# Kernel tuning notes

Hardware: AMD Instinct MI355X
Metric: run time of the kernel (lower is better)

Reference implementation:

```python
import jax, jax.numpy as jnp
import numpy as np

D_MODEL = 1024
D_FF = 4096
N_EXPERTS = 8
TOP_K = 2
GATE_TEMP = 1.0
LOAD_BALANCE_WEIGHT = 0.01


def setup_inputs() -> dict:
    key = jax.random.key(0)
    ks = jax.random.split(key, 6)
    B, S = 4, 2048
    x = jax.random.normal(ks[0], (B, S, D_MODEL), dtype=jnp.float32)
    # gate: nn.Linear(d_model, n_experts, bias=False), weight ~ N(0, 0.1)
    gate_w = 0.1 * jax.random.normal(ks[1], (N_EXPERTS, D_MODEL), dtype=jnp.float32)
    # stacked expert weights (stored as [in, out] for x @ W)
    s1 = 1.0 / np.sqrt(D_MODEL)
    s2 = 1.0 / np.sqrt(D_FF)
    W1 = jax.random.uniform(ks[2], (N_EXPERTS, D_MODEL, D_FF), jnp.float32, -s1, s1)
    b1 = jax.random.uniform(ks[3], (N_EXPERTS, D_FF), jnp.float32, -s1, s1)
    W2 = jax.random.uniform(ks[4], (N_EXPERTS, D_FF, D_MODEL), jnp.float32, -s2, s2)
    b2 = jax.random.uniform(ks[5], (N_EXPERTS, D_MODEL), jnp.float32, -s2, s2)
    return {"x": x, "gate_w": gate_w, "W1": W1, "b1": b1, "W2": W2, "b2": b2}


def reference(x, gate_w, W1, b1, W2, b2):
    B, S, D = x.shape
    E = gate_w.shape[0]
    xf = x.reshape(-1, D)                                  # [N, D]
    logits = (xf @ gate_w.T) / GATE_TEMP                   # [N, E]
    gate_probs = jax.nn.softmax(logits, axis=-1)           # [N, E]
    topk_probs, topk_idx = jax.lax.top_k(gate_probs, TOP_K)
    topk_probs = topk_probs / jnp.sum(topk_probs, axis=-1, keepdims=True)
    # per-token combine weight for each expert: [N, E]
    combine = jnp.einsum("nk,nke->ne", topk_probs,
                         jax.nn.one_hot(topk_idx, E, dtype=xf.dtype))
    out = jnp.zeros_like(xf)
    for e in range(E):  # fixed small loop over experts (structurally distinct weights)
        h = jax.nn.gelu(xf @ W1[e] + b1[e], approximate=False)  # [N, d_ff]
        out = out + combine[:, e:e + 1] * (h @ W2[e] + b2[e])
    out = out.reshape(B, S, D)
    # auxiliary load-balance loss (faithful: softmax probs > 0 almost surely)
    prob_mean = jnp.mean(gate_probs, axis=0)
    tokens_per_expert = jnp.mean((gate_probs > 0).astype(xf.dtype), axis=0)
    aux_loss = jnp.sum(prob_mean * tokens_per_expert) * E * LOAD_BALANCE_WEIGHT
    return out, aux_loss
```

## Files before the change

### kernel.cpp

```cpp
#include <hip/hip_runtime.h>
#include <cstdint>

typedef unsigned short u16;
typedef __attribute__((ext_vector_type(8))) __bf16 bf16x8;
typedef __attribute__((ext_vector_type(4))) float f32x4;

#define NTOK 8192
#define DM   1024
#define DFF  4096
#define NE   8
#define NT_MAX 136

typedef const __attribute__((address_space(1))) unsigned gl_u32;
typedef __attribute__((address_space(3))) unsigned lds_u32;

static __device__ __forceinline__ u16 f2bf(float f) {
    union { float f; unsigned u; } v; v.f = f;
    unsigned r = v.u + 0x7fffu + ((v.u >> 16) & 1u);
    return (u16)(r >> 16);
}

__global__ __launch_bounds__(256) void transpose_cvt_kernel(const float* __restrict__ W,
                                                            u16* __restrict__ WT,
                                                            int K, int F) {
    __shared__ float tile[64][33];
    size_t eo = (size_t)blockIdx.z * K * F;
    const float* src = W + eo;
    u16* dst = WT + eo;
    int k0 = blockIdx.y * 64, f0 = blockIdx.x * 32;
    int tid = threadIdx.x;
    {
        int rk = tid >> 2, cf = (tid & 3) * 8;
        const float* s = src + (size_t)(k0 + rk) * F + f0 + cf;
        f32x4 v0 = *(const f32x4*)(s);
        f32x4 v1 = *(const f32x4*)(s + 4);
#pragma unroll
        for (int i = 0; i < 4; i++) { tile[rk][cf + i] = v0[i]; tile[rk][cf + 4 + i] = v1[i]; }
    }
    __syncthreads();
    {
        int f = tid >> 3, kq = (tid & 7) * 8;
        union { ushort4 h[2]; uint4 q; } o;
#pragma unroll
        for (int i = 0; i < 8; i++) {
            u16 b = f2bf(tile[kq + i][f]);
            ((u16*)&o)[i] = b;
        }
        *(uint4*)(dst + (size_t)(f0 + f) * K + k0 + kq) = o.q;
    }
}

__global__ __launch_bounds__(256) void gate_kernel(const float* __restrict__ x,
                                                   const float* __restrict__ gw,
                                                   u16* __restrict__ xb,
                                                   int* __restrict__ cnt,
                                                   float* __restrict__ psum,
                                                   float* __restrict__ indsum,
                                                   int* __restrict__ list,
                                                   float* __restrict__ wgt,
                                                   int4* __restrict__ tokIE,
                                                   float2* __restrict__ tokW) {
    __shared__ float s_psum[NE], s_ind[NE];
    __shared__ int s_cnt[NE], s_base[NE];
    __shared__ int s_tok[NE][32];
    __shared__ float s_wgt[NE][32];
    __shared__ int s_e1[32], s_p1[32], s_e2[32], s_p2[32];
    __shared__ float s_w1[32], s_w2[32];
    int tid = threadIdx.x, lane = tid & 63, wid = tid >> 6;
    if (tid < NE) { s_psum[tid] = 0.f; s_ind[tid] = 0.f; s_cnt[tid] = 0; }
    __syncthreads();
#pragma unroll 1
    for (int it = 0; it < 8; it++) {
        int t = blockIdx.x * 32 + wid * 8 + it;
        const float* xr = x + (size_t)t * DM;
        float xv[16];
#pragma unroll
        for (int i = 0; i < 4; i++) {
            f32x4 v = *(const f32x4*)(xr + i * 256 + lane * 4);
            xv[4 * i + 0] = v[0]; xv[4 * i + 1] = v[1];
            xv[4 * i + 2] = v[2]; xv[4 * i + 3] = v[3];
            ushort4 o;
            o.x = f2bf(v[0]); o.y = f2bf(v[1]); o.z = f2bf(v[2]); o.w = f2bf(v[3]);
            *(ushort4*)(xb + (size_t)t * DM + i * 256 + lane * 4) = o;
        }
        float p[NE];
#pragma unroll
        for (int e = 0; e < NE; e++) {
            const float* gr = gw + (size_t)e * DM;
            float d = 0.f;
#pragma unroll
            for (int i = 0; i < 4; i++) {
                f32x4 g = *(const f32x4*)(gr + i * 256 + lane * 4);
                d += xv[4 * i] * g[0] + xv[4 * i + 1] * g[1]
                   + xv[4 * i + 2] * g[2] + xv[4 * i + 3] * g[3];
            }
#pragma unroll
            for (int off = 32; off; off >>= 1) d += __shfl_xor(d, off);
            p[e] = d;
        }
        float m = p[0];
#pragma unroll
        for (int e = 1; e < NE; e++) m = fmaxf(m, p[e]);
        float s = 0.f;
#pragma unroll
        for (int e = 0; e < NE; e++) { p[e] = expf(p[e] - m); s += p[e]; }
        float inv = 1.f / s;
#pragma unroll
        for (int e = 0; e < NE; e++) p[e] *= inv;
        int i1 = 0; float p1 = p[0];
#pragma unroll
        for (int e = 1; e < NE; e++) if (p[e] > p1) { p1 = p[e]; i1 = e; }
        int i2 = (i1 == 0) ? 1 : 0; float p2 = p[i2];
#pragma unroll
        for (int e = 0; e < NE; e++) if (e != i1 && p[e] > p2) { p2 = p[e]; i2 = e; }
        float wnorm = 1.f / (p1 + p2);
        if (lane == 0) {
#pragma unroll
            for (int e = 0; e < NE; e++) {
                atomicAdd(&s_psum[e], p[e]);
                atomicAdd(&s_ind[e], (p[e] > 0.f) ? 1.f : 0.f);
            }
            int pos1 = atomicAdd(&s_cnt[i1], 1);
            s_tok[i1][pos1] = t; s_wgt[i1][pos1] = p1 * wnorm;
            int pos2 = atomicAdd(&s_cnt[i2], 1);
            s_tok[i2][pos2] = t; s_wgt[i2][pos2] = p2 * wnorm;
            int sl = wid * 8 + it;
            s_e1[sl] = i1; s_p1[sl] = pos1; s_w1[sl] = p1 * wnorm;
            s_e2[sl] = i2; s_p2[sl] = pos2; s_w2[sl] = p2 * wnorm;
        }
    }
    __syncthreads();
    if (tid < NE) {
        s_base[tid] = atomicAdd(&cnt[tid], s_cnt[tid]);
        atomicAdd(&psum[tid], s_psum[tid]);
        atomicAdd(&indsum[tid], s_ind[tid]);
    }
    __syncthreads();
    for (int idx = tid; idx < NE * 32; idx += 256) {
        int e = idx >> 5, j = idx & 31;
        if (j < s_cnt[e]) {
            list[e * NTOK + s_base[e] + j] = s_tok[e][j];
            wgt[e * NTOK + s_base[e] + j] = s_wgt[e][j];
        }
    }
    if (tid < 32) {
        int t = blockIdx.x * 32 + tid;
        int e1 = s_e1[tid], e2 = s_e2[tid];
        tokIE[t] = make_int4(e1, s_base[e1] + s_p1[tid], e2, s_base[e2] + s_p2[tid]);
        tokW[t] = make_float2(s_w1[tid], s_w2[tid]);
    }
}

__global__ void finalize_kernel(const float* __restrict__ psum,
                                const float* __restrict__ indsum,
                                const int* __restrict__ cnt,
                                int* __restrict__ baseArr,
                                int* __restrict__ tileE,
                                int* __restrict__ tileM0,
                                int* __restrict__ nTiles,
                                float* __restrict__ out_aux) {
    if (threadIdx.x == 0) {
        float a = 0.f; int b = 0, nt = 0;
        for (int e = 0; e < NE; e++) {
            a += (psum[e] * (1.f / NTOK)) * (indsum[e] * (1.f / NTOK));
            baseArr[e] = b; b += cnt[e];
            int mt = (cnt[e] + 127) >> 7;
            for (int i = 0; i < mt; i++) { tileE[nt] = e; tileM0[nt] = i; nt++; }
        }
        nTiles[0] = nt;
        out_aux[0] = a * (float)NE * 0.01f;
    }
}

template <int KDIM, int EPI>
__global__ __launch_bounds__(256, 4) void gemm_kernel(const u16* __restrict__ A,
                                                      const u16* __restrict__ BT,
                                                      const float* __restrict__ bias,
                                                      const int* __restrict__ list,
                                                      const float* __restrict__ wgt,
                                                      const int* __restrict__ cnt,
                                                      const int* __restrict__ base,
                                                      const int* __restrict__ tileE,
                                                      const int* __restrict__ tileM0,
                                                      const int* __restrict__ nTiles,
                                                      u16* __restrict__ h_out,
                                                      float* __restrict__ out) {
    constexpr int NCOL = (EPI == 1) ? DFF : DM;
    constexpr int NY = NCOL / 128;
    constexpr int NT = KDIM / 64;
    constexpr int BAND = 4 * NY;
    int nwg = gridDim.x;
    int q = nwg >> 3, r = nwg & 7;
    int xcd = blockIdx.x & 7, idx0 = blockIdx.x >> 3;
    int wg = (xcd < r ? xcd * (q + 1) : r * (q + 1) + (xcd - r) * q) + idx0;
    int band = wg / BAND, ib = wg - band * BAND;
    int ny = ib >> 2;
    int t = band * 4 + (ib & 3);
    if (t >= nTiles[0]) return;
    int e = tileE[t];
    int m0 = tileM0[t] << 7;
    int M = cnt[e];
    int hb = base[e];
    int n0 = ny * 128;
    const int* le = list + e * NTOK;
    const float* we = wgt + e * NTOK;
    const u16* Bte = BT + (size_t)e * NCOL * KDIM;
    const float* be = bias + (size_t)e * NCOL;

    __shared__ __attribute__((aligned(16))) u16 lA[128 * 64];
    __shared__ __attribute__((aligned(16))) u16 lB[128 * 64];

    int tid = threadIdx.x;
    int lane = tid & 63, wid = tid >> 6;
    int wr = wid >> 1, wc = wid & 1;
    int r16 = lane & 15, hi = lane >> 4;
    int r8 = r16 & 7;

    const u16* aG[4]; const u16* bG[4]; int lofs[4];
#pragma unroll
    for (int qq = 0; qq < 4; qq++) {
        int lin = qq * 256 + tid;
        int row = lin >> 3, j = lin & 7;
        int js = j ^ (row & 7);
        lofs[qq] = lin * 8;
        int pos = m0 + row; if (pos > M - 1) pos = M - 1;
        size_t arow = (EPI == 1) ? (size_t)le[pos] : (size_t)(hb + pos);
        aG[qq] = A + arow * KDIM + js * 8;
        bG[qq] = Bte + (size_t)(n0 + row) * KDIM + js * 8;
    }

#define STAGE(k0)                                                                   \
    do {                                                                            \
        _Pragma("unroll")                                                           \
        for (int qq = 0; qq < 4; qq++) {                                            \
            __builtin_amdgcn_global_load_lds((gl_u32*)(aG[qq] + (k0)),              \
                (lds_u32*)(lA + lofs[qq]), 16, 0, 0);                               \
            __builtin_amdgcn_global_load_lds((gl_u32*)(bG[qq] + (k0)),              \
                (lds_u32*)(lB + lofs[qq]), 16, 0, 0);                               \
        }                                                                           \
    } while (0)

    f32x4 acc[4][4];
#pragma unroll
    for (int m = 0; m < 4; m++)
#pragma unroll
        for (int n = 0; n < 4; n++) acc[m][n] = (f32x4){0.f, 0.f, 0.f, 0.f};

    STAGE(0);

#pragma unroll 1
    for (int tI = 0; tI < NT; ++tI) {
        asm volatile("s_waitcnt vmcnt(0)" ::: "memory");
        __builtin_amdgcn_s_barrier();
#pragma unroll
        for (int kk = 0; kk < 2; kk++) {
            bf16x8 aF[4], bF[4];
            int ch = ((kk << 2) | hi) ^ r8;
#pragma unroll
            for (int m = 0; m < 4; m++)
                aF[m] = *(const bf16x8*)(lA + ((wr * 64 + m * 16 + r16) << 6) + (ch << 3));
#pragma unroll
            for (int n = 0; n < 4; n++)
                bF[n] = *(const bf16x8*)(lB + ((wc * 64 + n * 16 + r16) << 6) + (ch << 3));
            __builtin_amdgcn_s_setprio(1);
#pragma unroll
            for (int m = 0; m < 4; m++)
#pragma unroll
                for (int n = 0; n < 4; n++)
                    acc[m][n] = __builtin_amdgcn_mfma_f32_16x16x32_bf16(aF[m], bF[n], acc[m][n], 0, 0, 0);
            __builtin_amdgcn_s_setprio(0);
        }
        asm volatile("s_waitcnt lgkmcnt(0)" ::: "memory");
        __builtin_amdgcn_s_barrier();
        if (tI + 1 < NT) STAGE((tI + 1) * 64);
    }
#undef STAGE

#pragma unroll
    for (int m = 0; m < 4; m++) {
        int pr = m0 + wr * 64 + m * 16 + hi * 4;
#pragma unroll
        for (int n = 0; n < 4; n++) {
            int f = n0 + wc * 64 + n * 16 + r16;
#pragma unroll
            for (int j = 0; j < 4; j++) {
                int p = pr + j;
                if (p < M) {
                    if constexpr (EPI == 1) {
                        float v = acc[m][n][j] + be[f];
                        float ex = __expf(v * (1.5957691216f + 0.0713548162f * v * v));
                        v = v - v / (ex + 1.0f);
                        h_out[(size_t)(hb + p) * DFF + f] = f2bf(v);
                    } else if constexpr (EPI == 2) {
                        out[(size_t)(hb + p) * DM + f] = acc[m][n][j];
                    } else {
                        atomicAdd(out + (size_t)le[p] * DM + f,
                                  we[p] * (acc[m][n][j] + be[f]));
                    }
                }
            }
        }
    }
}

__global__ __launch_bounds__(256) void combine_kernel(const float* __restrict__ pairOut,
                                                      const float* __restrict__ b2,
                                                      const int4* __restrict__ tokIE,
                                                      const float2* __restrict__ tokW,
                                                      const int* __restrict__ baseArr,
                                                      float* __restrict__ out) {
    int t = blockIdx.x;
    int c = threadIdx.x * 4;
    int4 ie = tokIE[t];
    float2 w = tokW[t];
    int s1 = baseArr[ie.x] + ie.y, s2 = baseArr[ie.z] + ie.w;
    f32x4 v1 = *(const f32x4*)(pairOut + (size_t)s1 * DM + c);
    f32x4 v2 = *(const f32x4*)(pairOut + (size_t)s2 * DM + c);
    f32x4 g1 = *(const f32x4*)(b2 + (size_t)ie.x * DM + c);
    f32x4 g2 = *(const f32x4*)(b2 + (size_t)ie.z * DM + c);
    f32x4 res = w.x * (v1 + g1) + w.y * (v2 + g2);
    *(f32x4*)(out + (size_t)t * DM + c) = res;
}

extern "C" void kernel_launch(void* const* d_in, const int* in_sizes, int n_in,
                              void* d_out, int out_size, void* d_ws, size_t ws_size,
                              hipStream_t stream) {
    const float* x  = (const float*)d_in[0];
    const float* gw = (const float*)d_in[1];
    const float* W1 = (const float*)d_in[2];
    const float* b1 = (const float*)d_in[3];
    const float* W2 = (const float*)d_in[4];
    const float* b2 = (const float*)d_in[5];
    float* out = (float*)d_out;

    char* ws = (char*)d_ws;
    size_t o_xb   = 0;
    size_t o_w1t  = (size_t)16 << 20;
    size_t o_w2t  = o_w1t + ((size_t)64 << 20);
    size_t o_h    = o_w2t + ((size_t)64 << 20);
    size_t o_pair = o_h + ((size_t)128 << 20);
    size_t ctrl_sz = (size_t)1 << 20;
    bool pair_path = ws_size >= o_pair + ((size_t)64 << 20) + ctrl_sz;
    size_t o_ctrl = pair_path ? (o_pair + ((size_t)64 << 20)) : o_pair;

    u16* xb   = (u16*)(ws + o_xb);
    u16* w1t  = (u16*)(ws + o_w1t);
    u16* w2t  = (u16*)(ws + o_w2t);
    u16* h    = (u16*)(ws + o_h);
    float* pairOut = (float*)(ws + o_pair);
    char* ctrl = ws + o_ctrl;
    int*    cnt     = (int*)ctrl;
    float*  psum    = (float*)(ctrl + 32);
    float*  indsum  = (float*)(ctrl + 64);
    int*    baseArr = (int*)(ctrl + 96);
    int*    list    = (int*)(ctrl + 192);
    float*  wgt     = (float*)(ctrl + 192 + 262144);
    int4*   tokIE   = (int4*)(ctrl + 192 + 524288);
    float2* tokW    = (float2*)(ctrl + 192 + 655360);
    int*    tileE   = (int*)(ctrl + 192 + 720896);
    int*    tileM0  = (int*)(ctrl + 192 + 724992);
    int*    nTiles  = (int*)(ctrl + 192 + 729088);

    (void)hipMemsetAsync(ctrl, 0, 192, stream);
    if (!pair_path)
        (void)hipMemsetAsync(d_out, 0, (size_t)out_size * sizeof(float), stream);

    transpose_cvt_kernel<<<dim3(DFF / 32, DM / 64, NE), 256, 0, stream>>>(W1, w1t, DM, DFF);
    transpose_cvt_kernel<<<dim3(DM / 32, DFF / 64, NE), 256, 0, stream>>>(W2, w2t, DFF, DM);
    gate_kernel<<<NTOK / 32, 256, 0, stream>>>(x, gw, xb, cnt, psum, indsum, list, wgt, tokIE, tokW);
    finalize_kernel<<<1, 64, 0, stream>>>(psum, indsum, cnt, baseArr, tileE, tileM0, nTiles,
                                          out + (size_t)NTOK * DM);

    gemm_kernel<DM, 1><<<dim3(NT_MAX * (DFF / 128)), 256, 0, stream>>>(
        xb, w1t, b1, list, wgt, cnt, baseArr, tileE, tileM0, nTiles, h, nullptr);
    if (pair_path) {
        gemm_kernel<DFF, 2><<<dim3(NT_MAX * (DM / 128)), 256, 0, stream>>>(
            h, w2t, b2, list, wgt, cnt, baseArr, tileE, tileM0, nTiles, nullptr, pairOut);
        combine_kernel<<<NTOK, 256, 0, stream>>>(pairOut, b2, tokIE, tokW, baseArr, out);
    } else {
        gemm_kernel<DFF, 3><<<dim3(NT_MAX * (DM / 128)), 256, 0, stream>>>(
            h, w2t, b2, list, wgt, cnt, baseArr, tileE, tileM0, nTiles, nullptr, out);
    }
}
```

Measured before the change: 535.3 us.

## Split second expert GEMM along K into two halves and sum in combine

The down-projection GEMM is split-K by two: each tile is handled by two workgroups covering half of the 4096-long reduction, writing to separate partial buffers. The combine kernel adds both partials before applying bias and routing weights. This doubles the number of workgroups for the second GEMM, which otherwise has relatively few tiles for the GPU. The cost is an extra partial-output buffer (reusing the W1-transpose workspace region) plus extra reads in combine.

New measurement: 537.8 us. No clear change (+0.5%).

```diff
diff --git a/kernel.cpp b/kernel.cpp
--- a/kernel.cpp
+++ b/kernel.cpp
@@ -172,7 +172,7 @@
     }
 }
 
-template <int KDIM, int EPI>
+template <int KSTRIDE, int KLEN, int EPI>
 __global__ __launch_bounds__(256, 4) void gemm_kernel(const u16* __restrict__ A,
                                                       const u16* __restrict__ BT,
                                                       const float* __restrict__ bias,
@@ -184,15 +184,18 @@
                                                       const int* __restrict__ tileM0,
                                                       const int* __restrict__ nTiles,
                                                       u16* __restrict__ h_out,
-                                                      float* __restrict__ out) {
+                                                      float* __restrict__ out,
+                                                      float* __restrict__ out2) {
     constexpr int NCOL = (EPI == 1) ? DFF : DM;
     constexpr int NY = NCOL / 128;
-    constexpr int NT = KDIM / 64;
+    constexpr int NT = KLEN / 64;
     constexpr int BAND = 4 * NY;
     int nwg = gridDim.x;
     int q = nwg >> 3, r = nwg & 7;
     int xcd = blockIdx.x & 7, idx0 = blockIdx.x >> 3;
     int wg = (xcd < r ? xcd * (q + 1) : r * (q + 1) + (xcd - r) * q) + idx0;
+    int kh = 0;
+    if constexpr (EPI == 2) { kh = wg & 1; wg >>= 1; }
     int band = wg / BAND, ib = wg - band * BAND;
     int ny = ib >> 2;
     int t = band * 4 + (ib & 3);
@@ -202,9 +205,10 @@
     int M = cnt[e];
     int hb = base[e];
     int n0 = ny * 128;
+    int kOff = kh * KLEN;
     const int* le = list + e * NTOK;
     const float* we = wgt + e * NTOK;
-    const u16* Bte = BT + (size_t)e * NCOL * KDIM;
+    const u16* Bte = BT + (size_t)e * NCOL * KSTRIDE;
     const float* be = bias + (size_t)e * NCOL;
 
     __shared__ __attribute__((aligned(16))) u16 lA[128 * 64];
@@ -225,8 +229,8 @@
         lofs[qq] = lin * 8;
         int pos = m0 + row; if (pos > M - 1) pos = M - 1;
         size_t arow = (EPI == 1) ? (size_t)le[pos] : (size_t)(hb + pos);
-        aG[qq] = A + arow * KDIM + js * 8;
-        bG[qq] = Bte + (size_t)(n0 + row) * KDIM + js * 8;
+        aG[qq] = A + arow * KSTRIDE + kOff + js * 8;
+        bG[qq] = Bte + (size_t)(n0 + row) * KSTRIDE + kOff + js * 8;
     }
 
 #define STAGE(k0)                                                                   \
@@ -276,6 +280,7 @@
     }
 #undef STAGE
 
+    float* dst = (EPI == 2 && kh) ? out2 : out;
 #pragma unroll
     for (int m = 0; m < 4; m++) {
         int pr = m0 + wr * 64 + m * 16 + hi * 4;
@@ -292,7 +297,7 @@
                         v = v - v / (ex + 1.0f);
                         h_out[(size_t)(hb + p) * DFF + f] = f2bf(v);
                     } else if constexpr (EPI == 2) {
-                        out[(size_t)(hb + p) * DM + f] = acc[m][n][j];
+                        dst[(size_t)(hb + p) * DM + f] = acc[m][n][j];
                     } else {
                         atomicAdd(out + (size_t)le[p] * DM + f,
                                   we[p] * (acc[m][n][j] + be[f]));
@@ -303,7 +308,8 @@
     }
 }
 
-__global__ __launch_bounds__(256) void combine_kernel(const float* __restrict__ pairOut,
+__global__ __launch_bounds__(256) void combine_kernel(const float* __restrict__ pairA,
+                                                      const float* __restrict__ pairB,
                                                       const float* __restrict__ b2,
                                                       const int4* __restrict__ tokIE,
                                                       const float2* __restrict__ tokW,
@@ -314,11 +320,13 @@
     int4 ie = tokIE[t];
     float2 w = tokW[t];
     int s1 = baseArr[ie.x] + ie.y, s2 = baseArr[ie.z] + ie.w;
-    f32x4 v1 = *(const f32x4*)(pairOut + (size_t)s1 * DM + c);
-    f32x4 v2 = *(const f32x4*)(pairOut + (size_t)s2 * DM + c);
+    f32x4 a1 = *(const f32x4*)(pairA + (size_t)s1 * DM + c);
+    f32x4 b1v = *(const f32x4*)(pairB + (size_t)s1 * DM + c);
+    f32x4 a2 = *(const f32x4*)(pairA + (size_t)s2 * DM + c);
+    f32x4 b2v = *(const f32x4*)(pairB + (size_t)s2 * DM + c);
     f32x4 g1 = *(const f32x4*)(b2 + (size_t)ie.x * DM + c);
     f32x4 g2 = *(const f32x4*)(b2 + (size_t)ie.z * DM + c);
-    f32x4 res = w.x * (v1 + g1) + w.y * (v2 + g2);
+    f32x4 res = w.x * (a1 + b1v + g1) + w.y * (a2 + b2v + g2);
     *(f32x4*)(out + (size_t)t * DM + c) = res;
 }
 
@@ -347,7 +355,8 @@
     u16* w1t  = (u16*)(ws + o_w1t);
     u16* w2t  = (u16*)(ws + o_w2t);
     u16* h    = (u16*)(ws + o_h);
-    float* pairOut = (float*)(ws + o_pair);
+    float* pairA = (float*)(ws + o_pair);
+    float* pairB = (float*)(ws + o_w1t);
     char* ctrl = ws + o_ctrl;
     int*    cnt     = (int*)ctrl;
     float*  psum    = (float*)(ctrl + 32);
@@ -371,14 +380,14 @@
     finalize_kernel<<<1, 64, 0, stream>>>(psum, indsum, cnt, baseArr, tileE, tileM0, nTiles,
                                           out + (size_t)NTOK * DM);
 
-    gemm_kernel<DM, 1><<<dim3(NT_MAX * (DFF / 128)), 256, 0, stream>>>(
-        xb, w1t, b1, list, wgt, cnt, baseArr, tileE, tileM0, nTiles, h, nullptr);
+    gemm_kernel<DM, DM, 1><<<dim3(NT_MAX * (DFF / 128)), 256, 0, stream>>>(
+        xb, w1t, b1, list, wgt, cnt, baseArr, tileE, tileM0, nTiles, h, nullptr, nullptr);
     if (pair_path) {
-        gemm_kernel<DFF, 2><<<dim3(NT_MAX * (DM / 128)), 256, 0, stream>>>(
-            h, w2t, b2, list, wgt, cnt, baseArr, tileE, tileM0, nTiles, nullptr, pairOut);
-        combine_kernel<<<NTOK, 256, 0, stream>>>(pairOut, b2, tokIE, tokW, baseArr, out);
+        gemm_kernel<DFF, DFF / 2, 2><<<dim3(NT_MAX * (DM / 128) * 2), 256, 0, stream>>>(
+            h, w2t, b2, list, wgt, cnt, baseArr, tileE, tileM0, nTiles, nullptr, pairA, pairB);
+        combine_kernel<<<NTOK, 256, 0, stream>>>(pairA, pairB, b2, tokIE, tokW, baseArr, out);
     } else {
-        gemm_kernel<DFF, 3><<<dim3(NT_MAX * (DM / 128)), 256, 0, stream>>>(
-            h, w2t, b2, list, wgt, cnt, baseArr, tileE, tileM0, nTiles, nullptr, out);
-    }
-}
+        gemm_kernel<DFF, DFF, 3><<<dim3(NT_MAX * (DM / 128)), 256, 0, stream>>>(
+            h, w2t, b2, list, wgt, cnt, baseArr, tileE, tileM0, nTiles, nullptr, out, nullptr);
+    }
+}
```
